# Kernel tuning notes

Hardware: AMD Instinct MI355X
Metric: run time of the kernel (lower is better)

## Reference

```python
import jax, jax.numpy as jnp
import numpy as np

NUM_LEVELS = 16
LEVEL_DIM = 2
BASE_RES = 16
MAX_RES = 2048
HASHMAP_SIZE = 1 << 19
N_POINTS = 2000000

# Instant-NGP geometric progression of grid resolutions
_scale = np.exp2(np.log2(MAX_RES / BASE_RES) / (NUM_LEVELS - 1))
RESOLUTIONS = [int(np.ceil(BASE_RES * _scale ** l)) for l in range(NUM_LEVELS)]

# corner offsets of the unit cube, shape [8, 3]
_OFFS = np.stack(np.meshgrid([0, 1], [0, 1], [0, 1], indexing='ij'), -1).reshape(8, 3)
_PRIMES = np.array([1, 2654435761, 805459861], dtype=np.uint32)


def grid_encode(x, table):
    """x: [N,3] in [0,1]; table: [L, T, F] -> [N, L*F]."""
    offs = jnp.asarray(_OFFS, dtype=jnp.int32)          # [8,3]
    feats = []
    for l, res in enumerate(RESOLUTIONS):
        pos = x * (res - 1)                              # [N,3]
        pos_i = jnp.clip(jnp.floor(pos).astype(jnp.int32), 0, res - 2)
        frac = pos - pos_i.astype(pos.dtype)             # [N,3]
        corners = pos_i[:, None, :] + offs[None]         # [N,8,3]
        if res ** 3 <= HASHMAP_SIZE:
            # dense (collision-free) indexing for coarse levels
            idx = corners[..., 0] + res * (corners[..., 1] + res * corners[..., 2])
        else:
            # spatial hash: xor of coordinate * prime, mod table size
            c = corners.astype(jnp.uint32)
            h = (c[..., 0] * _PRIMES[0]) ^ (c[..., 1] * _PRIMES[1]) ^ (c[..., 2] * _PRIMES[2])
            idx = (h % jnp.uint32(HASHMAP_SIZE)).astype(jnp.int32)
        vals = table[l][idx]                             # [N,8,F] gather
        # multilinear interpolation weights per corner
        w = jnp.prod(jnp.where(offs[None].astype(bool), frac[:, None, :], 1.0 - frac[:, None, :]), axis=-1)  # [N,8]
        feats.append(jnp.einsum('nc,ncf->nf', w, vals))
    return jnp.concatenate(feats, axis=-1)               # [N, 32]


def setup_inputs() -> dict:
    key = jax.random.key(0)
    ks = jax.random.split(key, 6)
    x = jax.random.uniform(ks[0], (N_POINTS, 3), dtype=jnp.float32)
    table = jax.random.uniform(ks[1], (NUM_LEVELS, HASHMAP_SIZE, LEVEL_DIM),
                               dtype=jnp.float32, minval=-1e-4, maxval=1e-4)
    in_dim = NUM_LEVELS * LEVEL_DIM  # 32
    W1 = jax.random.normal(ks[2], (in_dim, 64), dtype=jnp.float32) / np.sqrt(in_dim)
    W2 = jax.random.normal(ks[3], (64, 64), dtype=jnp.float32) / 8.0
    W3 = jax.random.normal(ks[4], (64, 64), dtype=jnp.float32) / 8.0
    Wo = jax.random.normal(ks[5], (64, 1), dtype=jnp.float32) / 8.0
    z = lambda n: jnp.zeros((n,), dtype=jnp.float32)
    return {"x": x, "table": table, "W1": W1, "b1": z(64), "W2": W2, "b2": z(64),
            "W3": W3, "b3": z(64), "Wo": Wo, "bo": z(1)}


def reference(x, table, W1, b1, W2, b2, W3, b3, Wo, bo):
    h = grid_encode(x, table)                 # [N,32]
    h = jax.nn.relu(h @ W1 + b1)
    h = jax.nn.relu(h @ W2 + b2)
    h = jax.nn.relu(h @ W3 + b3)
    return h @ Wo + bo                        # [N,1]
```

## Files before the change

### kernel.cpp

```cpp
#include <hip/hip_runtime.h>
#include <hip/hip_fp16.h>
#include <cmath>
#include <cstdint>


#define HASH_SZ (1u << 19)
#define HMASK   (HASH_SZ - 1u)
#define PR2 2654435761u
#define PR3 805459861u

typedef float v2f __attribute__((ext_vector_type(2)));
typedef float v4f __attribute__((ext_vector_type(4)));
typedef v4f v4fu __attribute__((aligned(8)));
typedef v2f v2fu __attribute__((aligned(8)));
typedef short bf16x8 __attribute__((ext_vector_type(8)));
typedef float f32x4 __attribute__((ext_vector_type(4)));
typedef unsigned int u32;
typedef u32 u32x2 __attribute__((ext_vector_type(2)));
typedef u32 u32x4 __attribute__((ext_vector_type(4)));
typedef u32x4 u32x4u __attribute__((aligned(8)));

struct ResArr { int r[16]; };

__device__ __forceinline__ unsigned short bf16_rne(float f) {
    union { float f; unsigned u; } v; v.f = f;
    unsigned u = v.u;
    unsigned r = (u + 0x7fffu + ((u >> 16) & 1u)) >> 16;
    return (unsigned short)r;
}
__device__ __forceinline__ float bf16f(unsigned short h) {
    union { unsigned u; float f; } v; v.u = ((unsigned)h) << 16;
    return v.f;
}
__device__ __forceinline__ void split8(const float* x, bf16x8& hi, bf16x8& lo) {
    #pragma unroll
    for (int j = 0; j < 8; ++j) {
        union { float f; unsigned u; } v; v.f = x[j];
        const unsigned hu = v.u & 0xffff0000u;
        hi[j] = (short)(hu >> 16);
        union { unsigned u; float f; } hf; hf.u = hu;
        const float d = x[j] - hf.f;
        union { float f; unsigned u; } dv; dv.f = d;
        lo[j] = (short)((dv.u + 0x7fffu + ((dv.u >> 16) & 1u)) >> 16);
    }
}
__device__ __forceinline__ u32 rne16u(float f) {
    union { float f; u32 u; } v; v.f = f;
    return (v.u + 0x7fffu + ((v.u >> 16) & 1u)) >> 16;
}
__device__ __forceinline__ u32x2 pack_split2(float f0, float f1) {
    union { float f; u32 u; } a, b; a.f = f0; b.f = f1;
    const u32 h0 = a.u & 0xffff0000u, h1 = b.u & 0xffff0000u;
    union { u32 u; float f; } ha, hb; ha.u = h0; hb.u = h1;
    u32x2 r;
    r.x = (h0 >> 16) | h1;
    r.y = rne16u(f0 - ha.f) | (rne16u(f1 - hb.f) << 16);
    return r;
}

__device__ __forceinline__ u32 pkh(float f0, float f1) {
    const __half h0 = __float2half_rn(f0), h1 = __float2half_rn(f1);
    return (u32)__half_as_ushort(h0) | ((u32)__half_as_ushort(h1) << 16);
}
__device__ __forceinline__ v2f cvt2(u32 e) {
    __half2 h;
    *reinterpret_cast<u32*>(&h) = e;
    v2f r; r.x = __low2float(h); r.y = __high2float(h);
    return r;
}
__device__ __forceinline__ u32 sel4(u32x4 P, u32 k) {
    const u32 a = (k & 1u) ? P.y : P.x;
    const u32 b = (k & 1u) ? P.w : P.z;
    return (k & 2u) ? b : a;
}

__global__ __launch_bounds__(256, 8)
void cvt_table(const float* __restrict__ table, u32* __restrict__ tab16, int total)
{
    const int e0 = (blockIdx.x * 256 + threadIdx.x) * 4;
    if (e0 >= total) return;
    const v4f a = __builtin_nontemporal_load((const v4f*)(table + 2 * (size_t)e0));
    const v4f b = __builtin_nontemporal_load((const v4f*)(table + 2 * (size_t)e0 + 4));
    u32x4 o;
    o.x = pkh(a.x, a.y); o.y = pkh(a.z, a.w);
    o.z = pkh(b.x, b.y); o.w = pkh(b.z, b.w);
    *(u32x4*)(tab16 + e0) = o;
}

__device__ __forceinline__ void gather16_one(
    const u32* __restrict__ tab, int res, bool dense,
    float px, float py, float pz, float& A0, float& A1)
{
    const float rf = (float)(res - 1);
    const float fx = px * rf, fy = py * rf, fz = pz * rf;
    int ix = (int)floorf(fx), iy = (int)floorf(fy), iz = (int)floorf(fz);
    ix = min(max(ix, 0), res - 2);
    iy = min(max(iy, 0), res - 2);
    iz = min(max(iz, 0), res - 2);
    const float tx = fx - (float)ix, ty = fy - (float)iy, tz = fz - (float)iz;
    const float sx = 1.f - tx, sy = 1.f - ty, sz = 1.f - tz;
    float a0 = 0.f, a1 = 0.f;

    if (dense) {
        const int b0 = ix + res * (iy + res * iz);
        #pragma unroll
        for (int c = 0; c < 4; ++c) {
            const int dy = c >> 1, dz = c & 1;
            const u32 idx0 = (u32)(b0 + res * dy + res * res * dz);
            const u32x4u Pv = *(const u32x4u*)(tab + (idx0 & ~1u));
            const bool hi = (idx0 & 1u) != 0u;
            const u32 e0 = hi ? Pv.y : Pv.x;
            const u32 e1 = hi ? Pv.z : Pv.y;
            const float wyz = (dy ? ty : sy) * (dz ? tz : sz);
            const float w0 = sx * wyz, w1 = tx * wyz;
            const v2f f0 = cvt2(e0), f1 = cvt2(e1);
            a0 = fmaf(w0, f0.x, a0); a1 = fmaf(w0, f0.y, a1);
            a0 = fmaf(w1, f1.x, a0); a1 = fmaf(w1, f1.y, a1);
        }
    } else {
        u32 i1a[4], k0[4];
        u32x4 P[4];
        #pragma unroll
        for (int c = 0; c < 4; ++c) {
            const int dy = c >> 1, dz = c & 1;
            const u32 r = (u32)(iy + dy) * PR2 ^ (u32)(iz + dz) * PR3;
            const u32 i0 = ((u32)ix ^ r) & HMASK;
            i1a[c] = ((u32)(ix + 1) ^ r) & HMASK;
            k0[c] = i0 & 3u;
            P[c] = *(const u32x4*)(tab + (i0 & ~3u));
        }
        const bool extra = ((ix & 3) == 3);
        u32 O[4];
        if (extra) {
            #pragma unroll
            for (int c = 0; c < 4; ++c) O[c] = tab[i1a[c]];
        } else {
            #pragma unroll
            for (int c = 0; c < 4; ++c) O[c] = 0u;
        }
        #pragma unroll
        for (int c = 0; c < 4; ++c) {
            const int dy = c >> 1, dz = c & 1;
            const u32 e0 = sel4(P[c], k0[c]);
            const u32 e1w = sel4(P[c], i1a[c] & 3u);
            const u32 e1 = extra ? O[c] : e1w;
            const float wyz = (dy ? ty : sy) * (dz ? tz : sz);
            const float w0 = sx * wyz, w1 = tx * wyz;
            const v2f f0 = cvt2(e0), f1 = cvt2(e1);
            a0 = fmaf(w0, f0.x, a0); a1 = fmaf(w0, f0.y, a1);
            a0 = fmaf(w1, f1.x, a0); a1 = fmaf(w1, f1.y, a1);
        }
    }
    A0 = a0; A1 = a1;
}

template<int NLEV>
__global__ __launch_bounds__(256, 8)
void encode16_k(const float* __restrict__ x, const u32* __restrict__ tab16,
                u32x2* __restrict__ featT, int n, int ns, int lb, ResArr rv)
{
    const int nth2 = gridDim.x * 512;
    for (int q = (blockIdx.x * 256 + threadIdx.x) * 2; q < n; q += nth2) {
        float p0x, p0y, p0z, p1x, p1y, p1z;
        const bool two = (q + 1 < n);
        if (two) {
            const v4fu a = __builtin_nontemporal_load((const v4fu*)(x + 3 * q));
            const v2f  b = __builtin_nontemporal_load((const v2fu*)(x + 3 * q + 4));
            p0x = a.x; p0y = a.y; p0z = a.z; p1x = a.w; p1y = b.x; p1z = b.y;
        } else {
            p0x = x[3 * q]; p0y = x[3 * q + 1]; p0z = x[3 * q + 2];
            p1x = p0x; p1y = p0y; p1z = p0z;
        }
        #pragma unroll
        for (int il = 0; il < NLEV; ++il) {
            const int l = lb + il;
            const int res = rv.r[l];
            const bool dense = ((long long)res * res * res <= (long long)HASH_SZ);
            const u32* tbl = tab16 + (size_t)l * HASH_SZ;
            float a00, a01, a10, a11;
            gather16_one(tbl, res, dense, p0x, p0y, p0z, a00, a01);
            gather16_one(tbl, res, dense, p1x, p1y, p1z, a10, a11);
            if (two) {
                const u32x2 e0 = pack_split2(a00, a01);
                const u32x2 e1 = pack_split2(a10, a11);
                u32x4 st; st.x = e0.x; st.y = e0.y; st.z = e1.x; st.w = e1.y;
                __builtin_nontemporal_store(st, (u32x4*)&featT[(size_t)l * ns + q]);
            } else {
                __builtin_nontemporal_store(pack_split2(a00, a01),
                                            &featT[(size_t)l * ns + q]);
            }
        }
    }
}

__device__ __forceinline__ void gather_one(
    const v2f* __restrict__ tbl, int res, bool dense,
    float px, float py, float pz, float& A0, float& A1)
{
    const float rf = (float)(res - 1);
    const float fx = px * rf, fy = py * rf, fz = pz * rf;
    int ix = (int)floorf(fx), iy = (int)floorf(fy), iz = (int)floorf(fz);
    ix = min(max(ix, 0), res - 2);
    iy = min(max(iy, 0), res - 2);
    iz = min(max(iz, 0), res - 2);
    const float tx = fx - (float)ix, ty = fy - (float)iy, tz = fz - (float)iz;
    const float sx = 1.f - tx, sy = 1.f - ty, sz = 1.f - tz;
    float a0 = 0.f, a1 = 0.f;

    if (dense) {
        const int b0 = ix + res * (iy + res * iz);
        v4fu P[4];
        #pragma unroll
        for (int c = 0; c < 4; ++c) {
            const int dy = c >> 1, dz = c & 1;
            P[c] = *(const v4fu*)((const float*)tbl + 2 * (b0 + res * dy + res * res * dz));
        }
        #pragma unroll
        for (int c = 0; c < 4; ++c) {
            const int dy = c >> 1, dz = c & 1;
            const float wyz = (dy ? ty : sy) * (dz ? tz : sz);
            const float w0 = sx * wyz, w1 = tx * wyz;
            a0 = fmaf(w0, P[c].x, a0); a1 = fmaf(w0, P[c].y, a1);
            a0 = fmaf(w1, P[c].z, a0); a1 = fmaf(w1, P[c].w, a1);
        }
    } else {
        uint32_t i0[4], i1[4];
        v4f P[4];
        #pragma unroll
        for (int c = 0; c < 4; ++c) {
            const int dy = c >> 1, dz = c & 1;
            const uint32_t r = (uint32_t)(iy + dy) * PR2 ^ (uint32_t)(iz + dz) * PR3;
            i0[c] = ((uint32_t)ix ^ r) & HMASK;
            i1[c] = ((uint32_t)(ix + 1) ^ r) & HMASK;
            P[c] = *(const v4f*)((const float*)tbl + 2 * (i0[c] & ~1u));
        }
        const bool odd = (ix & 1);
        v2f O[4];
        if (odd) {
            #pragma unroll
            for (int c = 0; c < 4; ++c) O[c] = tbl[i1[c]];
        } else {
            #pragma unroll
            for (int c = 0; c < 4; ++c) { v2f z = {0.f, 0.f}; O[c] = z; }
        }
        #pragma unroll
        for (int c = 0; c < 4; ++c) {
            const int dy = c >> 1, dz = c & 1;
            const bool hi = (i0[c] & 1);
            v2f c0, e;
            c0.x = hi ? P[c].z : P[c].x;  c0.y = hi ? P[c].w : P[c].y;
            e.x  = hi ? P[c].x : P[c].z;  e.y  = hi ? P[c].y : P[c].w;
            const v2f c1 = odd ? O[c] : e;
            const float wyz = (dy ? ty : sy) * (dz ? tz : sz);
            const float w0 = sx * wyz, w1 = tx * wyz;
            a0 = fmaf(w0, c0.x, a0); a1 = fmaf(w0, c0.y, a1);
            a0 = fmaf(w1, c1.x, a0); a1 = fmaf(w1, c1.y, a1);
        }
    }
    A0 = a0; A1 = a1;
}

template<int NLEV>
__global__ __launch_bounds__(256, 8)
void encode_k(const float* __restrict__ x, const float* __restrict__ table,
              u32x2* __restrict__ featT, int n, int lb, ResArr rv)
{
    const int nth2 = gridDim.x * 512;
    for (int q = (blockIdx.x * 256 + threadIdx.x) * 2; q < n; q += nth2) {
        float p0x, p0y, p0z, p1x, p1y, p1z;
        const bool two = (q + 1 < n);
        if (two) {
            const v4fu a = __builtin_nontemporal_load((const v4fu*)(x + 3 * q));
            const v2f  b = __builtin_nontemporal_load((const v2fu*)(x + 3 * q + 4));
            p0x = a.x; p0y = a.y; p0z = a.z; p1x = a.w; p1y = b.x; p1z = b.y;
        } else {
            p0x = x[3 * q]; p0y = x[3 * q + 1]; p0z = x[3 * q + 2];
            p1x = p0x; p1y = p0y; p1z = p0z;
        }
        #pragma unroll
        for (int il = 0; il < NLEV; ++il) {
            const int l = lb + il;
            const int res = rv.r[l];
            const bool dense = ((long long)res * res * res <= (long long)HASH_SZ);
            const v2f* tbl = (const v2f*)table + (size_t)l * HASH_SZ;
            float a00, a01, a10, a11;
            gather_one(tbl, res, dense, p0x, p0y, p0z, a00, a01);
            gather_one(tbl, res, dense, p1x, p1y, p1z, a10, a11);
            if (two) {
                const u32x2 e0 = pack_split2(a00, a01);
                const u32x2 e1 = pack_split2(a10, a11);
                u32x4 st; st.x = e0.x; st.y = e0.y; st.z = e1.x; st.w = e1.y;
                __builtin_nontemporal_store(st, (u32x4*)&featT[(size_t)l * n + q]);
            } else {
                __builtin_nontemporal_store(pack_split2(a00, a01),
                                            &featT[(size_t)l * n + q]);
            }
        }
    }
}

__global__ void prep_weights(const float* __restrict__ W1,
                             const float* __restrict__ W2,
                             const float* __restrict__ W3,
                             unsigned short* __restrict__ wb)
{
    const int tid = threadIdx.x;
    const int nb = tid >> 6, lane = tid & 63;
    const int l15 = lane & 15, q = lane >> 4;
    #pragma unroll
    for (int j = 0; j < 8; ++j) {
        const float v = W1[(q * 8 + j) * 64 + nb * 16 + l15];
        const unsigned short h = bf16_rne(v);
        wb[(nb * 64 + lane) * 8 + j] = h;
        wb[2048 + (nb * 64 + lane) * 8 + j] = bf16_rne(v - bf16f(h));
    }
    #pragma unroll
    for (int kb = 0; kb < 2; ++kb) {
        #pragma unroll
        for (int j = 0; j < 8; ++j) {
            const int row = kb * 32 + q * 8 + j;
            const int idx = ((kb * 4 + nb) * 64 + lane) * 8 + j;
            float v = W2[row * 64 + nb * 16 + l15];
            unsigned short h = bf16_rne(v);
            wb[4096 + idx] = h;
            wb[8192 + idx] = bf16_rne(v - bf16f(h));
            v = W3[row * 64 + nb * 16 + l15];
            h = bf16_rne(v);
            wb[12288 + idx] = h;
            wb[16384 + idx] = bf16_rne(v - bf16f(h));
        }
    }
}

__global__ __launch_bounds__(256, 4)
void mlp_mfma(const u32x2* __restrict__ featT,
              const unsigned short* __restrict__ wb,
              const float* __restrict__ b1, const float* __restrict__ b2,
              const float* __restrict__ b3,
              const float* __restrict__ Wo, const float* __restrict__ bo,
              float* __restrict__ out, int n, int ns)
{
    const int wave = threadIdx.x >> 6;
    const int lane = threadIdx.x & 63;
    const int l15 = lane & 15, quad = lane >> 4;
    const int p0 = (blockIdx.x * 4 + wave) * 32;
    if (p0 >= n) return;

    bf16x8 bh[2], bl[2];
    #pragma unroll
    for (int t = 0; t < 2; ++t) {
        const int p = p0 + t * 16 + l15;
        const int pl = (p < n) ? p : (n - 1);
        u32x4 hw, lw;
        #pragma unroll
        for (int jj = 0; jj < 4; ++jj) {
            const u32x2 v = featT[(size_t)(quad * 4 + jj) * ns + pl];
            hw[jj] = v.x; lw[jj] = v.y;
        }
        bh[t] = *(bf16x8*)&hw;
        bl[t] = *(bf16x8*)&lw;
    }

    f32x4 acc[2][4];
    #pragma unroll
    for (int nb = 0; nb < 4; ++nb) {
        const bf16x8 wh = *(const bf16x8*)(wb + (nb * 64 + lane) * 8);
        const bf16x8 wl = *(const bf16x8*)(wb + 2048 + (nb * 64 + lane) * 8);
        const f32x4 bv = *(const f32x4*)(b1 + nb * 16 + quad * 4);
        #pragma unroll
        for (int t = 0; t < 2; ++t) {
            f32x4 c = bv;
            c = __builtin_amdgcn_mfma_f32_16x16x32_bf16(wh, bl[t], c, 0, 0, 0);
            c = __builtin_amdgcn_mfma_f32_16x16x32_bf16(wl, bh[t], c, 0, 0, 0);
            c = __builtin_amdgcn_mfma_f32_16x16x32_bf16(wh, bh[t], c, 0, 0, 0);
            acc[t][nb] = c;
        }
    }

    #pragma unroll
    for (int layer = 0; layer < 2; ++layer) {
        bf16x8 nh[2][2], nl[2][2];
        #pragma unroll
        for (int t = 0; t < 2; ++t) {
            #pragma unroll
            for (int kb = 0; kb < 2; ++kb) {
                float v[8];
                #pragma unroll
                for (int rr = 0; rr < 4; ++rr) {
                    float xq = fmaxf(acc[t][2 * kb][rr],     0.f);
                    float yq = fmaxf(acc[t][2 * kb + 1][rr], 0.f);
                    asm("v_permlane32_swap_b32 %0, %1" : "+v"(xq), "+v"(yq));
                    asm("v_permlane16_swap_b32 %0, %1" : "+v"(xq), "+v"(yq));
                    v[rr]     = xq;
                    v[4 + rr] = yq;
                }
                split8(v, nh[t][kb], nl[t][kb]);
            }
        }
        const int base_h = layer ? 12288 : 4096;
        const int base_l = layer ? 16384 : 8192;
        const float* __restrict__ bias = layer ? b3 : b2;
        #pragma unroll
        for (int nb = 0; nb < 4; ++nb) {
            const f32x4 bv = *(const f32x4*)(bias + nb * 16 + quad * 4);
            f32x4 c[2];
            #pragma unroll
            for (int t = 0; t < 2; ++t) c[t] = bv;
            #pragma unroll
            for (int kb = 0; kb < 2; ++kb) {
                const int idx = ((kb * 4 + nb) * 64 + lane) * 8;
                const bf16x8 wh = *(const bf16x8*)(wb + base_h + idx);
                const bf16x8 wl = *(const bf16x8*)(wb + base_l + idx);
                #pragma unroll
                for (int t = 0; t < 2; ++t) {
                    c[t] = __builtin_amdgcn_mfma_f32_16x16x32_bf16(wh, nl[t][kb], c[t], 0, 0, 0);
                    c[t] = __builtin_amdgcn_mfma_f32_16x16x32_bf16(wl, nh[t][kb], c[t], 0, 0, 0);
                    c[t] = __builtin_amdgcn_mfma_f32_16x16x32_bf16(wh, nh[t][kb], c[t], 0, 0, 0);
                }
            }
            #pragma unroll
            for (int t = 0; t < 2; ++t) acc[t][nb] = c[t];
        }
    }

    float part[2];
    #pragma unroll
    for (int t = 0; t < 2; ++t) {
        float s = 0.f;
        #pragma unroll
        for (int nb = 0; nb < 4; ++nb) {
            const f32x4 wo4 = *(const f32x4*)(Wo + nb * 16 + quad * 4);
            #pragma unroll
            for (int r = 0; r < 4; ++r)
                s = fmaf(fmaxf(acc[t][nb][r], 0.f), wo4[r], s);
        }
        part[t] = s;
    }
    #pragma unroll
    for (int t = 0; t < 2; ++t) {
        part[t] += __shfl_xor(part[t], 16, 64);
        part[t] += __shfl_xor(part[t], 32, 64);
    }
    if (quad == 0) {
        const float b = bo[0];
        #pragma unroll
        for (int t = 0; t < 2; ++t) {
            const int po = p0 + t * 16 + l15;
            if (po < n) out[po] = part[t] + b;
        }
    }
}

__global__ __launch_bounds__(256, 3)
void mlp_forward(const u32x2* __restrict__ featT,
                 const float* __restrict__ W1, const float* __restrict__ b1,
                 const float* __restrict__ W2, const float* __restrict__ b2,
                 const float* __restrict__ W3, const float* __restrict__ b3,
                 const float* __restrict__ Wo, const float* __restrict__ bo,
                 float* __restrict__ out, int n)
{
    const int p = blockIdx.x * 256 + threadIdx.x;
    if (p >= n) return;
    const v2f z2 = {0.f, 0.f};
    v2f A[32], B[32];
    #pragma unroll
    for (int jq = 0; jq < 16; ++jq) {
        const v4f b = *(const v4f*)(b1 + 4 * jq);
        A[2 * jq] = b.xy; A[2 * jq + 1] = b.zw;
    }
    #pragma unroll
    for (int l = 0; l < 16; ++l) {
        const u32x2 e = __builtin_nontemporal_load(&featT[(size_t)l * n + p]);
        union { u32 u; float f; } h0, h1, l0, l1;
        h0.u = e.x << 16; h1.u = e.x & 0xffff0000u;
        l0.u = e.y << 16; l1.u = e.y & 0xffff0000u;
        v2f f; f.x = h0.f + l0.f; f.y = h1.f + l1.f;
        const v4f* w0 = (const v4f*)(W1 + (size_t)(2 * l) * 64);
        const v4f* w1 = (const v4f*)(W1 + (size_t)(2 * l + 1) * 64);
        const v2f hh0 = {f.x, f.x}, hh1 = {f.y, f.y};
        #pragma unroll
        for (int jq = 0; jq < 16; ++jq) {
            const v4f wa = w0[jq];
            A[2 * jq]     = __builtin_elementwise_fma(hh0, wa.xy, A[2 * jq]);
            A[2 * jq + 1] = __builtin_elementwise_fma(hh0, wa.zw, A[2 * jq + 1]);
        }
        #pragma unroll
        for (int jq = 0; jq < 16; ++jq) {
            const v4f wb2 = w1[jq];
            A[2 * jq]     = __builtin_elementwise_fma(hh1, wb2.xy, A[2 * jq]);
            A[2 * jq + 1] = __builtin_elementwise_fma(hh1, wb2.zw, A[2 * jq + 1]);
        }
    }
    #pragma unroll
    for (int j = 0; j < 32; ++j) A[j] = __builtin_elementwise_max(A[j], z2);
    #pragma unroll
    for (int jq = 0; jq < 16; ++jq) {
        const v4f b = *(const v4f*)(b2 + 4 * jq);
        B[2 * jq] = b.xy; B[2 * jq + 1] = b.zw;
    }
    #pragma unroll
    for (int k = 0; k < 64; ++k) {
        const float hv = A[k >> 1][k & 1];
        const v2f h = {hv, hv};
        const v4f* w = (const v4f*)(W2 + (size_t)k * 64);
        #pragma unroll
        for (int jq = 0; jq < 16; ++jq) {
            const v4f wa = w[jq];
            B[2 * jq]     = __builtin_elementwise_fma(h, wa.xy, B[2 * jq]);
            B[2 * jq + 1] = __builtin_elementwise_fma(h, wa.zw, B[2 * jq + 1]);
        }
    }
    #pragma unroll
    for (int j = 0; j < 32; ++j) B[j] = __builtin_elementwise_max(B[j], z2);
    #pragma unroll
    for (int jq = 0; jq < 16; ++jq) {
        const v4f b = *(const v4f*)(b3 + 4 * jq);
        A[2 * jq] = b.xy; A[2 * jq + 1] = b.zw;
    }
    #pragma unroll
    for (int k = 0; k < 64; ++k) {
        const float hv = B[k >> 1][k & 1];
        const v2f h = {hv, hv};
        const v4f* w = (const v4f*)(W3 + (size_t)k * 64);
        #pragma unroll
        for (int jq = 0; jq < 16; ++jq) {
            const v4f wa = w[jq];
            A[2 * jq]     = __builtin_elementwise_fma(h, wa.xy, A[2 * jq]);
            A[2 * jq + 1] = __builtin_elementwise_fma(h, wa.zw, A[2 * jq + 1]);
        }
    }
    v2f o2 = z2;
    #pragma unroll
    for (int jq = 0; jq < 16; ++jq) {
        const v4f wa = *(const v4f*)(Wo + 4 * jq);
        o2 = __builtin_elementwise_fma(__builtin_elementwise_max(A[2 * jq], z2),     wa.xy, o2);
        o2 = __builtin_elementwise_fma(__builtin_elementwise_max(A[2 * jq + 1], z2), wa.zw, o2);
    }
    out[p] = o2.x + o2.y + bo[0];
}

__global__ __launch_bounds__(256, 2)
void hashpinn_fused(const float* __restrict__ x,
                    const float* __restrict__ table,
                    const float* __restrict__ W1, const float* __restrict__ b1,
                    const float* __restrict__ W2, const float* __restrict__ b2,
                    const float* __restrict__ W3, const float* __restrict__ b3,
                    const float* __restrict__ Wo, const float* __restrict__ bo,
                    float* __restrict__ out, int n, ResArr rv)
{
    const int p = blockIdx.x * 256 + threadIdx.x;
    if (p >= n) return;
    const float px = x[3*p+0], py = x[3*p+1], pz = x[3*p+2];
    float feat[32];
    #pragma unroll
    for (int l = 0; l < 16; ++l) {
        const int res = rv.r[l];
        const float rf = (float)(res - 1);
        const float fx = px*rf, fy = py*rf, fz = pz*rf;
        int ix=(int)floorf(fx), iy=(int)floorf(fy), iz=(int)floorf(fz);
        ix=min(max(ix,0),res-2); iy=min(max(iy,0),res-2); iz=min(max(iz,0),res-2);
        const float tx=fx-(float)ix, ty=fy-(float)iy, tz=fz-(float)iz;
        const float sx=1.f-tx, sy=1.f-ty, sz=1.f-tz;
        const float2* tbl=(const float2*)table+(size_t)l*HASH_SZ;
        const bool dense=((long long)res*res*res<=(long long)HASH_SZ);
        float a0=0.f, a1=0.f;
        #pragma unroll
        for (int c=0;c<8;++c){
            const uint32_t cx=(uint32_t)(ix+((c>>2)&1));
            const uint32_t cy=(uint32_t)(iy+((c>>1)&1));
            const uint32_t cz=(uint32_t)(iz+(c&1));
            uint32_t idx = dense ? cx+(uint32_t)res*(cy+(uint32_t)res*cz)
                                 : ((cx*1u ^ cy*PR2 ^ cz*PR3)&HMASK);
            const float2 v=tbl[idx];
            const float w=(((c>>2)&1)?tx:sx)*(((c>>1)&1)?ty:sy)*((c&1)?tz:sz);
            a0=fmaf(w,v.x,a0); a1=fmaf(w,v.y,a1);
        }
        feat[2*l]=a0; feat[2*l+1]=a1;
    }
    float A[64], B[64];
    #pragma unroll
    for (int j=0;j<64;++j) A[j]=b1[j];
    #pragma unroll
    for (int k=0;k<32;++k){ const float h=feat[k];
        #pragma unroll
        for (int j=0;j<64;++j) A[j]=fmaf(h,W1[k*64+j],A[j]); }
    #pragma unroll 1
    for (int it=0;it<2;++it){
        const float* W = it?W3:W2; const float* bb = it?b3:b2;
        #pragma unroll
        for (int j=0;j<64;++j){ A[j]=fmaxf(A[j],0.f); B[j]=bb[j]; }
        #pragma unroll
        for (int k=0;k<64;++k){ const float h=A[k];
            #pragma unroll
            for (int j=0;j<64;++j) B[j]=fmaf(h,W[k*64+j],B[j]); }
        #pragma unroll
        for (int j=0;j<64;++j) A[j]=B[j];
    }
    float o=bo[0];
    #pragma unroll
    for (int j=0;j<64;++j) o=fmaf(fmaxf(A[j],0.f),Wo[j],o);
    out[p]=o;
}

static inline void launch_encode16(int nlev, const float* x, const u32* tab16,
                                   u32x2* featT, int n, int ns, int lb,
                                   const ResArr& rv, hipStream_t stream) {
    const dim3 g((n + 511) / 512), b(256);
    switch (nlev) {
        case 1: hipLaunchKernelGGL(encode16_k<1>, g, b, 0, stream, x, tab16, featT, n, ns, lb, rv); break;
        case 2: hipLaunchKernelGGL(encode16_k<2>, g, b, 0, stream, x, tab16, featT, n, ns, lb, rv); break;
        case 3: hipLaunchKernelGGL(encode16_k<3>, g, b, 0, stream, x, tab16, featT, n, ns, lb, rv); break;
        case 4: hipLaunchKernelGGL(encode16_k<4>, g, b, 0, stream, x, tab16, featT, n, ns, lb, rv); break;
        case 5: hipLaunchKernelGGL(encode16_k<5>, g, b, 0, stream, x, tab16, featT, n, ns, lb, rv); break;
        case 6: hipLaunchKernelGGL(encode16_k<6>, g, b, 0, stream, x, tab16, featT, n, ns, lb, rv); break;
        case 7: hipLaunchKernelGGL(encode16_k<7>, g, b, 0, stream, x, tab16, featT, n, ns, lb, rv); break;
        default: hipLaunchKernelGGL(encode16_k<8>, g, b, 0, stream, x, tab16, featT, n, ns, lb, rv); break;
    }
}

static inline void launch_encode(int nlev, const float* x, const float* table,
                                 u32x2* featT, int n, int lb, const ResArr& rv,
                                 hipStream_t stream) {
    const dim3 g(4096), b(256);
    switch (nlev) {
        case 1: hipLaunchKernelGGL(encode_k<1>, g, b, 0, stream, x, table, featT, n, lb, rv); break;
        case 2: hipLaunchKernelGGL(encode_k<2>, g, b, 0, stream, x, table, featT, n, lb, rv); break;
        case 3: hipLaunchKernelGGL(encode_k<3>, g, b, 0, stream, x, table, featT, n, lb, rv); break;
        case 4: hipLaunchKernelGGL(encode_k<4>, g, b, 0, stream, x, table, featT, n, lb, rv); break;
        case 5: hipLaunchKernelGGL(encode_k<5>, g, b, 0, stream, x, table, featT, n, lb, rv); break;
        case 6: hipLaunchKernelGGL(encode_k<6>, g, b, 0, stream, x, table, featT, n, lb, rv); break;
        case 7: hipLaunchKernelGGL(encode_k<7>, g, b, 0, stream, x, table, featT, n, lb, rv); break;
        default: hipLaunchKernelGGL(encode_k<8>, g, b, 0, stream, x, table, featT, n, lb, rv); break;
    }
}

extern "C" void kernel_launch(void* const* d_in, const int* in_sizes, int n_in,
                              void* d_out, int out_size, void* d_ws, size_t ws_size,
                              hipStream_t stream) {
    const float* x     = (const float*)d_in[0];
    const float* table = (const float*)d_in[1];
    const float* W1    = (const float*)d_in[2];
    const float* b1    = (const float*)d_in[3];
    const float* W2    = (const float*)d_in[4];
    const float* b2    = (const float*)d_in[5];
    const float* W3    = (const float*)d_in[6];
    const float* b3    = (const float*)d_in[7];
    const float* Wo    = (const float*)d_in[8];
    const float* bo    = (const float*)d_in[9];
    float* out = (float*)d_out;

    const int n = in_sizes[0] / 3;

    ResArr rv;
    const double scale = std::exp2(std::log2(2048.0 / 16.0) / 15.0);
    for (int l = 0; l < 16; ++l)
        rv.r[l] = (int)std::ceil(16.0 * std::pow(scale, (double)l));

    int dense_end = 0;
    while (dense_end < 16) {
        long long r = rv.r[dense_end];
        if (r * r * r <= (long long)HASH_SZ) ++dense_end; else break;
    }
    if (dense_end > 8) dense_end = 8;

    const size_t wb_bytes = 20480 * sizeof(unsigned short);
    const size_t tab16_bytes = (size_t)16 * HASH_SZ * sizeof(u32);
    const int total_entries = 16 * (int)HASH_SZ;

    int h0 = ((n + 1) / 2 + 1) & ~1;
    if (h0 > n) h0 = n;
    const int h1 = n - h0;
    const int ns0 = (h0 + 1) & ~1;
    const int ns1 = (h1 + 1) & ~1;
    const int nsmax = ns0 > ns1 ? ns0 : ns1;
    const size_t feat_half_bytes = (size_t)nsmax * 16 * sizeof(u32x2);

    const size_t feat_bytes = (size_t)n * 16 * sizeof(u32x2);

    if (ws_size >= feat_half_bytes + wb_bytes + tab16_bytes) {
        u32x2* featT = (u32x2*)d_ws;
        unsigned short* wb = (unsigned short*)((char*)d_ws + feat_half_bytes);
        u32* tab16 = (u32*)((char*)d_ws + feat_half_bytes + wb_bytes);

        hipLaunchKernelGGL(prep_weights, dim3(1), dim3(256), 0, stream, W1, W2, W3, wb);
        hipLaunchKernelGGL(cvt_table, dim3(8192), dim3(256), 0, stream,
                           table, tab16, total_entries);

        #pragma unroll
        for (int half = 0; half < 2; ++half) {
            const int off = half ? h0 : 0;
            const int nh  = half ? h1 : h0;
            const int ns  = half ? ns1 : ns0;
            if (nh <= 0) continue;
            const float* xh = x + (size_t)3 * off;

            if (dense_end > 0)
                launch_encode16(dense_end, xh, tab16, featT, nh, ns, 0, rv, stream);
            for (int l = dense_end; l < 16; ++l)
                launch_encode16(1, xh, tab16, featT, nh, ns, l, rv, stream);

            const int nblocks = (nh + 127) / 128;
            hipLaunchKernelGGL(mlp_mfma, dim3(nblocks), dim3(256), 0, stream,
                               featT, wb, b1, b2, b3, Wo, bo, out + off, nh, ns);
        }
    } else if (ws_size >= feat_bytes + wb_bytes) {
        u32x2* featT = (u32x2*)d_ws;
        unsigned short* wb = (unsigned short*)((char*)d_ws + feat_bytes);

        hipLaunchKernelGGL(prep_weights, dim3(1), dim3(256), 0, stream, W1, W2, W3, wb);

        if (dense_end > 0)
            launch_encode(dense_end, x, table, featT, n, 0, rv, stream);
        for (int l = dense_end; l < 16; ++l)
            launch_encode(1, x, table, featT, n, l, rv, stream);

        const int nblocks = (n + 127) / 128;
        hipLaunchKernelGGL(mlp_mfma, dim3(nblocks), dim3(256), 0, stream,
                           featT, wb, b1, b2, b3, Wo, bo, out, n, n);
    } else if (ws_size >= feat_bytes) {
        u32x2* featT = (u32x2*)d_ws;
        if (dense_end > 0)
            launch_encode(dense_end, x, table, featT, n, 0, rv, stream);
        for (int l = dense_end; l < 16; ++l)
            launch_encode(1, x, table, featT, n, l, rv, stream);
        hipLaunchKernelGGL(mlp_forward, dim3((n + 255) / 256), dim3(256), 0, stream,
                           featT, W1, b1, W2, b2, W3, b3, Wo, bo, out, n);
    } else {
        hipLaunchKernelGGL(hashpinn_fused, dim3((n + 255) / 256), dim3(256), 0, stream,
                           x, table, W1, b1, W2, b2, W3, b3, Wo, bo, out, n, rv);
    }
}
```

Measured before the change: 981.8 us.

## Fuse dense-level gathers into MLP kernel and widen hash gather window to 8

The dense, collision-free coarse levels are now interpolated directly inside the MLP kernel from the fp16 table, so they no longer go through a separate encode kernel and a featT round trip, and the feature buffer shrinks to hashed levels only. Hashed levels use a dedicated kernel that loads a 32-byte window of 8 entries per corner pair, so the extra load for the x+1 neighbour is needed only when ix%8==7. Launch bounds for the hashed encoder drop to 4 waves per EU. The cost is heavier per-lane work in the MLP kernel, which may hurt its occupancy, and twice the bytes fetched per hashed corner load.

```diff
diff --git a/kernel.cpp b/kernel.cpp
--- a/kernel.cpp
+++ b/kernel.cpp
@@ -68,10 +68,14 @@
     v2f r; r.x = __low2float(h); r.y = __high2float(h);
     return r;
 }
-__device__ __forceinline__ u32 sel4(u32x4 P, u32 k) {
-    const u32 a = (k & 1u) ? P.y : P.x;
-    const u32 b = (k & 1u) ? P.w : P.z;
-    return (k & 2u) ? b : a;
+__device__ __forceinline__ u32 sel8(u32x4 lo, u32x4 hi, u32 k) {
+    const u32 a = (k & 1u) ? lo.y : lo.x;
+    const u32 b = (k & 1u) ? lo.w : lo.z;
+    const u32 c = (k & 1u) ? hi.y : hi.x;
+    const u32 d = (k & 1u) ? hi.w : hi.z;
+    const u32 e = (k & 2u) ? b : a;
+    const u32 f = (k & 2u) ? d : c;
+    return (k & 4u) ? f : e;
 }
 
 __global__ __launch_bounds__(256, 8)
@@ -87,8 +91,8 @@
     *(u32x4*)(tab16 + e0) = o;
 }
 
-__device__ __forceinline__ void gather16_one(
-    const u32* __restrict__ tab, int res, bool dense,
+__device__ __forceinline__ void gather16h(
+    const u32* __restrict__ tab, int res,
     float px, float py, float pz, float& A0, float& A1)
 {
     const float rf = (float)(res - 1);
@@ -101,63 +105,77 @@
     const float sx = 1.f - tx, sy = 1.f - ty, sz = 1.f - tz;
     float a0 = 0.f, a1 = 0.f;
 
-    if (dense) {
-        const int b0 = ix + res * (iy + res * iz);
-        #pragma unroll
-        for (int c = 0; c < 4; ++c) {
-            const int dy = c >> 1, dz = c & 1;
-            const u32 idx0 = (u32)(b0 + res * dy + res * res * dz);
-            const u32x4u Pv = *(const u32x4u*)(tab + (idx0 & ~1u));
-            const bool hi = (idx0 & 1u) != 0u;
-            const u32 e0 = hi ? Pv.y : Pv.x;
-            const u32 e1 = hi ? Pv.z : Pv.y;
-            const float wyz = (dy ? ty : sy) * (dz ? tz : sz);
-            const float w0 = sx * wyz, w1 = tx * wyz;
-            const v2f f0 = cvt2(e0), f1 = cvt2(e1);
-            a0 = fmaf(w0, f0.x, a0); a1 = fmaf(w0, f0.y, a1);
-            a0 = fmaf(w1, f1.x, a0); a1 = fmaf(w1, f1.y, a1);
-        }
+    u32 i1a[4], k0[4];
+    u32x4 lo[4], hi[4];
+    #pragma unroll
+    for (int c = 0; c < 4; ++c) {
+        const int dy = c >> 1, dz = c & 1;
+        const u32 r = (u32)(iy + dy) * PR2 ^ (u32)(iz + dz) * PR3;
+        const u32 i0 = ((u32)ix ^ r) & HMASK;
+        i1a[c] = ((u32)(ix + 1) ^ r) & HMASK;
+        k0[c] = i0 & 7u;
+        const u32 base = i0 & ~7u;
+        lo[c] = *(const u32x4*)(tab + base);
+        hi[c] = *(const u32x4*)(tab + base + 4);
+    }
+    const bool extra = ((ix & 7) == 7);
+    u32 O[4];
+    if (extra) {
+        #pragma unroll
+        for (int c = 0; c < 4; ++c) O[c] = tab[i1a[c]];
     } else {
-        u32 i1a[4], k0[4];
-        u32x4 P[4];
-        #pragma unroll
-        for (int c = 0; c < 4; ++c) {
-            const int dy = c >> 1, dz = c & 1;
-            const u32 r = (u32)(iy + dy) * PR2 ^ (u32)(iz + dz) * PR3;
-            const u32 i0 = ((u32)ix ^ r) & HMASK;
-            i1a[c] = ((u32)(ix + 1) ^ r) & HMASK;
-            k0[c] = i0 & 3u;
-            P[c] = *(const u32x4*)(tab + (i0 & ~3u));
-        }
-        const bool extra = ((ix & 3) == 3);
-        u32 O[4];
-        if (extra) {
-            #pragma unroll
-            for (int c = 0; c < 4; ++c) O[c] = tab[i1a[c]];
-        } else {
-            #pragma unroll
-            for (int c = 0; c < 4; ++c) O[c] = 0u;
-        }
-        #pragma unroll
-        for (int c = 0; c < 4; ++c) {
-            const int dy = c >> 1, dz = c & 1;
-            const u32 e0 = sel4(P[c], k0[c]);
-            const u32 e1w = sel4(P[c], i1a[c] & 3u);
-            const u32 e1 = extra ? O[c] : e1w;
-            const float wyz = (dy ? ty : sy) * (dz ? tz : sz);
-            const float w0 = sx * wyz, w1 = tx * wyz;
-            const v2f f0 = cvt2(e0), f1 = cvt2(e1);
-            a0 = fmaf(w0, f0.x, a0); a1 = fmaf(w0, f0.y, a1);
-            a0 = fmaf(w1, f1.x, a0); a1 = fmaf(w1, f1.y, a1);
-        }
+        #pragma unroll
+        for (int c = 0; c < 4; ++c) O[c] = 0u;
+    }
+    #pragma unroll
+    for (int c = 0; c < 4; ++c) {
+        const int dy = c >> 1, dz = c & 1;
+        const u32 e0 = sel8(lo[c], hi[c], k0[c]);
+        const u32 e1w = sel8(lo[c], hi[c], i1a[c] & 7u);
+        const u32 e1 = extra ? O[c] : e1w;
+        const float wyz = (dy ? ty : sy) * (dz ? tz : sz);
+        const float w0 = sx * wyz, w1 = tx * wyz;
+        const v2f f0 = cvt2(e0), f1 = cvt2(e1);
+        a0 = fmaf(w0, f0.x, a0); a1 = fmaf(w0, f0.y, a1);
+        a0 = fmaf(w1, f1.x, a0); a1 = fmaf(w1, f1.y, a1);
     }
     A0 = a0; A1 = a1;
 }
 
-template<int NLEV>
-__global__ __launch_bounds__(256, 8)
-void encode16_k(const float* __restrict__ x, const u32* __restrict__ tab16,
-                u32x2* __restrict__ featT, int n, int ns, int lb, ResArr rv)
+__device__ __forceinline__ void gather16d(
+    const u32* __restrict__ tab, int res,
+    float px, float py, float pz, float& A0, float& A1)
+{
+    const float rf = (float)(res - 1);
+    const float fx = px * rf, fy = py * rf, fz = pz * rf;
+    int ix = (int)floorf(fx), iy = (int)floorf(fy), iz = (int)floorf(fz);
+    ix = min(max(ix, 0), res - 2);
+    iy = min(max(iy, 0), res - 2);
+    iz = min(max(iz, 0), res - 2);
+    const float tx = fx - (float)ix, ty = fy - (float)iy, tz = fz - (float)iz;
+    const float sx = 1.f - tx, sy = 1.f - ty, sz = 1.f - tz;
+    float a0 = 0.f, a1 = 0.f;
+    const int b0 = ix + res * (iy + res * iz);
+    #pragma unroll
+    for (int c = 0; c < 4; ++c) {
+        const int dy = c >> 1, dz = c & 1;
+        const u32 idx0 = (u32)(b0 + res * dy + res * res * dz);
+        const u32x4u Pv = *(const u32x4u*)(tab + (idx0 & ~1u));
+        const bool hh = (idx0 & 1u) != 0u;
+        const u32 e0 = hh ? Pv.y : Pv.x;
+        const u32 e1 = hh ? Pv.z : Pv.y;
+        const float wyz = (dy ? ty : sy) * (dz ? tz : sz);
+        const float w0 = sx * wyz, w1 = tx * wyz;
+        const v2f f0 = cvt2(e0), f1 = cvt2(e1);
+        a0 = fmaf(w0, f0.x, a0); a1 = fmaf(w0, f0.y, a1);
+        a0 = fmaf(w1, f1.x, a0); a1 = fmaf(w1, f1.y, a1);
+    }
+    A0 = a0; A1 = a1;
+}
+
+__global__ __launch_bounds__(256, 4)
+void encode16h_k(const float* __restrict__ x, const u32* __restrict__ tbl,
+                 u32x2* __restrict__ featT, int n, int ns, int slot, int res)
 {
     const int nth2 = gridDim.x * 512;
     for (int q = (blockIdx.x * 256 + threadIdx.x) * 2; q < n; q += nth2) {
@@ -171,24 +189,17 @@
             p0x = x[3 * q]; p0y = x[3 * q + 1]; p0z = x[3 * q + 2];
             p1x = p0x; p1y = p0y; p1z = p0z;
         }
-        #pragma unroll
-        for (int il = 0; il < NLEV; ++il) {
-            const int l = lb + il;
-            const int res = rv.r[l];
-            const bool dense = ((long long)res * res * res <= (long long)HASH_SZ);
-            const u32* tbl = tab16 + (size_t)l * HASH_SZ;
-            float a00, a01, a10, a11;
-            gather16_one(tbl, res, dense, p0x, p0y, p0z, a00, a01);
-            gather16_one(tbl, res, dense, p1x, p1y, p1z, a10, a11);
-            if (two) {
-                const u32x2 e0 = pack_split2(a00, a01);
-                const u32x2 e1 = pack_split2(a10, a11);
-                u32x4 st; st.x = e0.x; st.y = e0.y; st.z = e1.x; st.w = e1.y;
-                __builtin_nontemporal_store(st, (u32x4*)&featT[(size_t)l * ns + q]);
-            } else {
-                __builtin_nontemporal_store(pack_split2(a00, a01),
-                                            &featT[(size_t)l * ns + q]);
-            }
+        float a00, a01, a10, a11;
+        gather16h(tbl, res, p0x, p0y, p0z, a00, a01);
+        gather16h(tbl, res, p1x, p1y, p1z, a10, a11);
+        if (two) {
+            const u32x2 e0 = pack_split2(a00, a01);
+            const u32x2 e1 = pack_split2(a10, a11);
+            u32x4 st; st.x = e0.x; st.y = e0.y; st.z = e1.x; st.w = e1.y;
+            __builtin_nontemporal_store(st, (u32x4*)&featT[(size_t)slot * ns + q]);
+        } else {
+            __builtin_nontemporal_store(pack_split2(a00, a01),
+                                        &featT[(size_t)slot * ns + q]);
         }
     }
 }
@@ -333,12 +344,14 @@
 }
 
 __global__ __launch_bounds__(256, 4)
-void mlp_mfma(const u32x2* __restrict__ featT,
-              const unsigned short* __restrict__ wb,
-              const float* __restrict__ b1, const float* __restrict__ b2,
-              const float* __restrict__ b3,
-              const float* __restrict__ Wo, const float* __restrict__ bo,
-              float* __restrict__ out, int n, int ns)
+void mlp_mfma_f(const u32x2* __restrict__ featT,
+                const unsigned short* __restrict__ wb,
+                const float* __restrict__ b1, const float* __restrict__ b2,
+                const float* __restrict__ b3,
+                const float* __restrict__ Wo, const float* __restrict__ bo,
+                float* __restrict__ out, int n, int ns,
+                const float* __restrict__ xh, const u32* __restrict__ tab16,
+                ResArr rv, int de)
 {
     const int wave = threadIdx.x >> 6;
     const int lane = threadIdx.x & 63;
@@ -351,14 +364,26 @@
     for (int t = 0; t < 2; ++t) {
         const int p = p0 + t * 16 + l15;
         const int pl = (p < n) ? p : (n - 1);
-        u32x4 hw, lw;
+        const float px = xh[3 * pl], py = xh[3 * pl + 1], pz = xh[3 * pl + 2];
+        u32 hw[4], lw[4];
         #pragma unroll
         for (int jj = 0; jj < 4; ++jj) {
-            const u32x2 v = featT[(size_t)(quad * 4 + jj) * ns + pl];
-            hw[jj] = v.x; lw[jj] = v.y;
-        }
-        bh[t] = *(bf16x8*)&hw;
-        bl[t] = *(bf16x8*)&lw;
+            const int lvl = quad * 4 + jj;
+            if (lvl < de) {
+                float a0, a1;
+                gather16d(tab16 + (size_t)lvl * HASH_SZ, rv.r[lvl], px, py, pz, a0, a1);
+                const u32x2 e = pack_split2(a0, a1);
+                hw[jj] = e.x; lw[jj] = e.y;
+            } else {
+                const u32x2 v = featT[(size_t)(lvl - de) * ns + pl];
+                hw[jj] = v.x; lw[jj] = v.y;
+            }
+        }
+        u32x4 hwv, lwv;
+        hwv.x = hw[0]; hwv.y = hw[1]; hwv.z = hw[2]; hwv.w = hw[3];
+        lwv.x = lw[0]; lwv.y = lw[1]; lwv.z = lw[2]; lwv.w = lw[3];
+        bh[t] = *(bf16x8*)&hwv;
+        bl[t] = *(bf16x8*)&lwv;
     }
 
     f32x4 acc[2][4];
@@ -451,6 +476,125 @@
     }
 }
 
+__global__ __launch_bounds__(256, 4)
+void mlp_mfma(const u32x2* __restrict__ featT,
+              const unsigned short* __restrict__ wb,
+              const float* __restrict__ b1, const float* __restrict__ b2,
+              const float* __restrict__ b3,
+              const float* __restrict__ Wo, const float* __restrict__ bo,
+              float* __restrict__ out, int n, int ns)
+{
+    const int wave = threadIdx.x >> 6;
+    const int lane = threadIdx.x & 63;
+    const int l15 = lane & 15, quad = lane >> 4;
+    const int p0 = (blockIdx.x * 4 + wave) * 32;
+    if (p0 >= n) return;
+
+    bf16x8 bh[2], bl[2];
+    #pragma unroll
+    for (int t = 0; t < 2; ++t) {
+        const int p = p0 + t * 16 + l15;
+        const int pl = (p < n) ? p : (n - 1);
+        u32x4 hw, lw;
+        #pragma unroll
+        for (int jj = 0; jj < 4; ++jj) {
+            const u32x2 v = featT[(size_t)(quad * 4 + jj) * ns + pl];
+            hw[jj] = v.x; lw[jj] = v.y;
+        }
+        bh[t] = *(bf16x8*)&hw;
+        bl[t] = *(bf16x8*)&lw;
+    }
+
+    f32x4 acc[2][4];
+    #pragma unroll
+    for (int nb = 0; nb < 4; ++nb) {
+        const bf16x8 wh = *(const bf16x8*)(wb + (nb * 64 + lane) * 8);
+        const bf16x8 wl = *(const bf16x8*)(wb + 2048 + (nb * 64 + lane) * 8);
+        const f32x4 bv = *(const f32x4*)(b1 + nb * 16 + quad * 4);
+        #pragma unroll
+        for (int t = 0; t < 2; ++t) {
+            f32x4 c = bv;
+            c = __builtin_amdgcn_mfma_f32_16x16x32_bf16(wh, bl[t], c, 0, 0, 0);
+            c = __builtin_amdgcn_mfma_f32_16x16x32_bf16(wl, bh[t], c, 0, 0, 0);
+            c = __builtin_amdgcn_mfma_f32_16x16x32_bf16(wh, bh[t], c, 0, 0, 0);
+            acc[t][nb] = c;
+        }
+    }
+
+    #pragma unroll
+    for (int layer = 0; layer < 2; ++layer) {
+        bf16x8 nh[2][2], nl[2][2];
+        #pragma unroll
+        for (int t = 0; t < 2; ++t) {
+            #pragma unroll
+            for (int kb = 0; kb < 2; ++kb) {
+                float v[8];
+                #pragma unroll
+                for (int rr = 0; rr < 4; ++rr) {
+                    float xq = fmaxf(acc[t][2 * kb][rr],     0.f);
+                    float yq = fmaxf(acc[t][2 * kb + 1][rr], 0.f);
+                    asm("v_permlane32_swap_b32 %0, %1" : "+v"(xq), "+v"(yq));
+                    asm("v_permlane16_swap_b32 %0, %1" : "+v"(xq), "+v"(yq));
+                    v[rr]     = xq;
+                    v[4 + rr] = yq;
+                }
+                split8(v, nh[t][kb], nl[t][kb]);
+            }
+        }
+        const int base_h = layer ? 12288 : 4096;
+        const int base_l = layer ? 16384 : 8192;
+        const float* __restrict__ bias = layer ? b3 : b2;
+        #pragma unroll
+        for (int nb = 0; nb < 4; ++nb) {
+            const f32x4 bv = *(const f32x4*)(bias + nb * 16 + quad * 4);
+            f32x4 c[2];
+            #pragma unroll
+            for (int t = 0; t < 2; ++t) c[t] = bv;
+            #pragma unroll
+            for (int kb = 0; kb < 2; ++kb) {
+                const int idx = ((kb * 4 + nb) * 64 + lane) * 8;
+                const bf16x8 wh = *(const bf16x8*)(wb + base_h + idx);
+                const bf16x8 wl = *(const bf16x8*)(wb + base_l + idx);
+                #pragma unroll
+                for (int t = 0; t < 2; ++t) {
+                    c[t] = __builtin_amdgcn_mfma_f32_16x16x32_bf16(wh, nl[t][kb], c[t], 0, 0, 0);
+                    c[t] = __builtin_amdgcn_mfma_f32_16x16x32_bf16(wl, nh[t][kb], c[t], 0, 0, 0);
+                    c[t] = __builtin_amdgcn_mfma_f32_16x16x32_bf16(wh, nh[t][kb], c[t], 0, 0, 0);
+                }
+            }
+            #pragma unroll
+            for (int t = 0; t < 2; ++t) acc[t][nb] = c[t];
+        }
+    }
+
+    float part[2];
+    #pragma unroll
+    for (int t = 0; t < 2; ++t) {
+        float s = 0.f;
+        #pragma unroll
+        for (int nb = 0; nb < 4; ++nb) {
+            const f32x4 wo4 = *(const f32x4*)(Wo + nb * 16 + quad * 4);
+            #pragma unroll
+            for (int r = 0; r < 4; ++r)
+                s = fmaf(fmaxf(acc[t][nb][r], 0.f), wo4[r], s);
+        }
+        part[t] = s;
+    }
+    #pragma unroll
+    for (int t = 0; t < 2; ++t) {
+        part[t] += __shfl_xor(part[t], 16, 64);
+        part[t] += __shfl_xor(part[t], 32, 64);
+    }
+    if (quad == 0) {
+        const float b = bo[0];
+        #pragma unroll
+        for (int t = 0; t < 2; ++t) {
+            const int po = p0 + t * 16 + l15;
+            if (po < n) out[po] = part[t] + b;
+        }
+    }
+}
+
 __global__ __launch_bounds__(256, 3)
 void mlp_forward(const u32x2* __restrict__ featT,
                  const float* __restrict__ W1, const float* __restrict__ b1,
@@ -600,22 +744,6 @@
     #pragma unroll
     for (int j=0;j<64;++j) o=fmaf(fmaxf(A[j],0.f),Wo[j],o);
     out[p]=o;
-}
-
-static inline void launch_encode16(int nlev, const float* x, const u32* tab16,
-                                   u32x2* featT, int n, int ns, int lb,
-                                   const ResArr& rv, hipStream_t stream) {
-    const dim3 g((n + 511) / 512), b(256);
-    switch (nlev) {
-        case 1: hipLaunchKernelGGL(encode16_k<1>, g, b, 0, stream, x, tab16, featT, n, ns, lb, rv); break;
-        case 2: hipLaunchKernelGGL(encode16_k<2>, g, b, 0, stream, x, tab16, featT, n, ns, lb, rv); break;
-        case 3: hipLaunchKernelGGL(encode16_k<3>, g, b, 0, stream, x, tab16, featT, n, ns, lb, rv); break;
-        case 4: hipLaunchKernelGGL(encode16_k<4>, g, b, 0, stream, x, tab16, featT, n, ns, lb, rv); break;
-        case 5: hipLaunchKernelGGL(encode16_k<5>, g, b, 0, stream, x, tab16, featT, n, ns, lb, rv); break;
-        case 6: hipLaunchKernelGGL(encode16_k<6>, g, b, 0, stream, x, tab16, featT, n, ns, lb, rv); break;
-        case 7: hipLaunchKernelGGL(encode16_k<7>, g, b, 0, stream, x, tab16, featT, n, ns, lb, rv); break;
-        default: hipLaunchKernelGGL(encode16_k<8>, g, b, 0, stream, x, tab16, featT, n, ns, lb, rv); break;
-    }
 }
 
 static inline void launch_encode(int nlev, const float* x, const float* table,
@@ -673,7 +801,8 @@
     const int ns0 = (h0 + 1) & ~1;
     const int ns1 = (h1 + 1) & ~1;
     const int nsmax = ns0 > ns1 ? ns0 : ns1;
-    const size_t feat_half_bytes = (size_t)nsmax * 16 * sizeof(u32x2);
+    const int nhashed = 16 - dense_end;
+    const size_t feat_half_bytes = (size_t)nsmax * nhashed * sizeof(u32x2);
 
     const size_t feat_bytes = (size_t)n * 16 * sizeof(u32x2);
 
@@ -686,22 +815,23 @@
         hipLaunchKernelGGL(cvt_table, dim3(8192), dim3(256), 0, stream,
                            table, tab16, total_entries);
 
-        #pragma unroll
         for (int half = 0; half < 2; ++half) {
             const int off = half ? h0 : 0;
             const int nh  = half ? h1 : h0;
             const int ns  = half ? ns1 : ns0;
             if (nh <= 0) continue;
             const float* xh = x + (size_t)3 * off;
-
-            if (dense_end > 0)
-                launch_encode16(dense_end, xh, tab16, featT, nh, ns, 0, rv, stream);
+            const dim3 ge((nh + 511) / 512), be(256);
+
             for (int l = dense_end; l < 16; ++l)
-                launch_encode16(1, xh, tab16, featT, nh, ns, l, rv, stream);
+                hipLaunchKernelGGL(encode16h_k, ge, be, 0, stream,
+                                   xh, tab16 + (size_t)l * HASH_SZ, featT,
+                                   nh, ns, l - dense_end, rv.r[l]);
 
             const int nblocks = (nh + 127) / 128;
-            hipLaunchKernelGGL(mlp_mfma, dim3(nblocks), dim3(256), 0, stream,
-                               featT, wb, b1, b2, b3, Wo, bo, out + off, nh, ns);
+            hipLaunchKernelGGL(mlp_mfma_f, dim3(nblocks), dim3(256), 0, stream,
+                               featT, wb, b1, b2, b3, Wo, bo, out + off, nh, ns,
+                               xh, tab16, rv, dense_end);
         }
     } else if (ws_size >= feat_bytes + wb_bytes) {
         u32x2* featT = (u32x2*)d_ws;
```

After: 1.096 ms. 11.7% more time.
